# Kernel optimization log

Hardware: AMD Instinct MI355X
Metric: run time of the kernel (lower is better)

The kernel has to match this reference:

```python
import jax, jax.numpy as jnp
import numpy as np

NUM_HEADS = 16
LN_EPS = 1e-5


def setup_inputs() -> dict:
    key = jax.random.key(0)
    ks = jax.random.split(key, 7)
    B, S, D = 4, 1024, 1024
    s_in = 1.0 / np.sqrt(D)
    return {
        "x": jax.random.normal(ks[0], (B, S, D), dtype=jnp.float32),
        # PyTorch MHA packed in-projection: [3D, D] weight, [3D] bias
        "w_qkv": jax.random.uniform(ks[1], (3 * D, D), dtype=jnp.float32, minval=-s_in, maxval=s_in),
        "b_qkv": jnp.zeros((3 * D,), dtype=jnp.float32),
        "w_out": jax.random.uniform(ks[2], (D, D), dtype=jnp.float32, minval=-s_in, maxval=s_in),
        "b_out": jnp.zeros((D,), dtype=jnp.float32),
        "ln_w": jnp.ones((D,), dtype=jnp.float32),
        "ln_b": jnp.zeros((D,), dtype=jnp.float32),
    }


def _layernorm(x, w, b):
    m = jnp.mean(x, axis=-1, keepdims=True)
    v = jnp.var(x, axis=-1, keepdims=True)
    return (x - m) * jax.lax.rsqrt(v + LN_EPS) * w + b


def reference(x, w_qkv, b_qkv, w_out, b_out, ln_w, ln_b):
    B, S, D = x.shape
    H = NUM_HEADS
    hd = D // H
    # packed QKV projection (torch: F.linear(x, w_qkv, b_qkv) then chunk)
    qkv = x @ w_qkv.T + b_qkv                      # [B, S, 3D]
    q, k, v = jnp.split(qkv, 3, axis=-1)
    q = q.reshape(B, S, H, hd).transpose(0, 2, 1, 3) * (hd ** -0.5)  # [B,H,S,hd]
    k = k.reshape(B, S, H, hd).transpose(0, 2, 1, 3)
    v = v.reshape(B, S, H, hd).transpose(0, 2, 1, 3)
    scores = jnp.einsum('bhqd,bhkd->bhqk', q, k)   # [B,H,S,S]
    attn = jax.nn.softmax(scores, axis=-1)
    ctx = jnp.einsum('bhqk,bhkd->bhqd', attn, v)   # [B,H,S,hd]
    ctx = ctx.transpose(0, 2, 1, 3).reshape(B, S, D)
    attn_out = ctx @ w_out.T + b_out
    # torch returns head-averaged weights (average_attn_weights=True)
    attn_weights = attn.mean(axis=1)               # [B,S,S]
    # dropout rate 0.0 -> identity; residual + LayerNorm
    y = _layernorm(x + attn_out, ln_w, ln_b)
    return y, attn_weights
```

## Files before the change

kernel.cpp:

```cpp
#include <hip/hip_runtime.h>
#include <cstdint>

typedef __bf16 bf16;
typedef __bf16 bf16x8 __attribute__((ext_vector_type(8)));
typedef __bf16 bf16x4 __attribute__((ext_vector_type(4)));
typedef float  f32x4  __attribute__((ext_vector_type(4)));

#define MFMA_BF16(a, b, c) __builtin_amdgcn_mfma_f32_16x16x32_bf16(a, b, c, 0, 0, 0)

#define WAITCNT_VM(n) asm volatile("s_waitcnt vmcnt(" #n ")" ::: "memory")
#define CFENCE()      asm volatile("" ::: "memory")

__device__ __forceinline__ void async_load16(const void* g, void* l) {
    __builtin_amdgcn_global_load_lds(
        (__attribute__((address_space(1))) uint32_t*)(uintptr_t)g,
        (__attribute__((address_space(3))) uint32_t*)(uint32_t)(uintptr_t)l,
        16, 0, 0);
}

__global__ void cvt3_kernel(const float* __restrict__ s0, bf16* __restrict__ d0, int n0,
                            const float* __restrict__ s1, bf16* __restrict__ d1, int n1) {
    int i = blockIdx.x * blockDim.x + threadIdx.x;
    const float* s; bf16* d; int j = i;
    if (j < n0) { s = s0; d = d0; }
    else { j -= n0; if (j >= n1) return; s = s1; d = d1; }
    float4 v = ((const float4*)s)[j];
    bf16x4 o;
    o[0] = (bf16)v.x; o[1] = (bf16)v.y; o[2] = (bf16)v.z; o[3] = (bf16)v.w;
    ((bf16x4*)d)[j] = o;
}

__global__ __launch_bounds__(256) void gemm_qkv_kernel(
    const bf16* __restrict__ A, const bf16* __restrict__ W,
    const float* __restrict__ bias,
    bf16* __restrict__ Qb, bf16* __restrict__ Kb, bf16* __restrict__ Vt)
{
    const int Kd = 1024;
    __shared__ __attribute__((aligned(16))) bf16 smem[6 * 128 * 32];
    bf16* const sA0 = smem;
    bf16* const sB0 = smem + 3 * 4096;
    int tid = threadIdx.x, lane = tid & 63, wid = tid >> 6;
    int flat = blockIdx.y * 24 + blockIdx.x;
    int xcd = flat & 7, local = flat >> 3;
    int n0 = (xcd * 3 + local % 3) * 128;
    int m0 = (local / 3) * 128;
    int srow = wid * 32 + (lane >> 2);
    int pchunk = lane & 3;
    int jchunk = pchunk ^ ((lane >> 3) & 3);
    const bf16* Ag = A + (size_t)(m0 + srow) * Kd + jchunk * 8;
    const bf16* Wg = W + (size_t)(n0 + srow) * Kd + jchunk * 8;
    int soff = srow * 32 + pchunk * 8;
    int wm = (wid & 1) * 64, wn = (wid >> 1) * 64;
    int lcol = lane & 15, quad = lane >> 4;
    int ckey = (lcol >> 1) & 3;
    f32x4 acc[4][4] = {};
#define STG_Q(buf, k0_) do { \
        async_load16(Ag + (k0_), sA0 + (buf) * 4096 + soff); \
        async_load16(Ag + (k0_) + 16 * Kd, sA0 + (buf) * 4096 + soff + 512); \
        async_load16(Wg + (k0_), sB0 + (buf) * 4096 + soff); \
        async_load16(Wg + (k0_) + 16 * Kd, sB0 + (buf) * 4096 + soff + 512); \
    } while (0)
    STG_Q(0, 0);
    STG_Q(1, 32);
    STG_Q(2, 64);
    int cur = 0;
    for (int it = 0; it < 32; ++it) {
        if (it < 30)      { WAITCNT_VM(8); }
        else if (it == 30){ WAITCNT_VM(4); }
        else              { WAITCNT_VM(0); }
        __builtin_amdgcn_s_barrier();
        CFENCE();
        const bf16* cA = sA0 + cur * 4096;
        const bf16* cB = sB0 + cur * 4096;
        bf16x8 af[4], bfr[4];
#pragma unroll
        for (int i = 0; i < 4; i++)
            af[i] = *(const bf16x8*)&cA[(wm + i * 16 + lcol) * 32 + (quad ^ ckey) * 8];
#pragma unroll
        for (int i = 0; i < 4; i++)
            bfr[i] = *(const bf16x8*)&cB[(wn + i * 16 + lcol) * 32 + (quad ^ ckey) * 8];
#pragma unroll
        for (int i = 0; i < 4; i++)
#pragma unroll
            for (int j = 0; j < 4; j++)
                acc[i][j] = MFMA_BF16(af[i], bfr[j], acc[i][j]);
        CFENCE();
        __builtin_amdgcn_s_barrier();
        if (it + 3 < 32) STG_Q(cur, (it + 3) * 32);
        cur = (cur == 2) ? 0 : cur + 1;
    }
#undef STG_Q
    const int LP = 136;
    bf16* sE = smem;
    int part = n0 >> 10;
    int h0 = (n0 & 1023) >> 6;
    int b = m0 >> 10, s0 = m0 & 1023;
    if (part == 2) {
#pragma unroll
        for (int j = 0; j < 4; j++) {
            float bv = bias[n0 + wn + j * 16 + lcol];
#pragma unroll
            for (int i = 0; i < 4; i++)
#pragma unroll
                for (int r = 0; r < 4; r++)
                    sE[(wn + j * 16 + lcol) * LP + (wm + i * 16 + quad * 4 + r)] = (bf16)(acc[i][j][r] + bv);
        }
        __syncthreads();
#pragma unroll
        for (int p = 0; p < 8; p++) {
            int c = p * 256 + tid;
            int nl = c >> 4, mc = (c & 15) * 8;
            int dd = nl & 63, h = h0 + (nl >> 6);
            *(bf16x8*)&Vt[(size_t)((b * 16 + h) * 64 + dd) * 1024 + s0 + mc] = *(const bf16x8*)&sE[nl * LP + mc];
        }
    } else {
        float scv = (part == 0) ? 0.125f : 1.0f;
        bf16* dst = (part == 0) ? Qb : Kb;
#pragma unroll
        for (int j = 0; j < 4; j++) {
            float bv = bias[n0 + wn + j * 16 + lcol];
#pragma unroll
            for (int i = 0; i < 4; i++)
#pragma unroll
                for (int r = 0; r < 4; r++)
                    sE[(wm + i * 16 + quad * 4 + r) * LP + (wn + j * 16 + lcol)] = (bf16)((acc[i][j][r] + bv) * scv);
        }
        __syncthreads();
#pragma unroll
        for (int p = 0; p < 8; p++) {
            int c = p * 256 + tid;
            int half = c >> 10, idx = c & 1023;
            int m = idx >> 3, nc = (idx & 7) * 8;
            *(bf16x8*)&dst[(size_t)((b * 16 + h0 + half) * 1024 + s0 + m) * 64 + nc] =
                *(const bf16x8*)&sE[m * LP + half * 64 + nc];
        }
    }
}

__global__ __launch_bounds__(512) void flash_kernel(
    const bf16* __restrict__ Qb, const bf16* __restrict__ Kb, const bf16* __restrict__ Vt,
    bf16* __restrict__ ctx, float* __restrict__ ml,
    const float* __restrict__ wof, bf16* __restrict__ wob)
{
    __shared__ bf16 sK[2][64 * 64];
    __shared__ bf16 sV[2][64 * 64];
    __shared__ bf16 pt[8][16 * 64];
    int tid = threadIdx.x, lane = tid & 63, wid = tid >> 6;
    int bx = blockIdx.x;
    if (bx >= 512) {
        int i = (bx - 512) * 512 + tid;
        float4 v = ((const float4*)wof)[i];
        bf16x4 o;
        o[0] = (bf16)v.x; o[1] = (bf16)v.y; o[2] = (bf16)v.z; o[3] = (bf16)v.w;
        ((bf16x4*)wob)[i] = o;
        return;
    }
    int orig = (bx & 7) * 64 + (bx >> 3);
    int qt = orig & 7;
    int h = (orig >> 3) & 15;
    int b = orig >> 7;
    int lcol = lane & 15, quad = lane >> 4;
    size_t base = (size_t)(b * 16 + h) * 65536;

    int q0 = qt * 128 + wid * 16;
    const bf16* qp = Qb + base + (size_t)(q0 + lcol) * 64 + quad * 8;
    bf16x8 a0 = *(const bf16x8*)qp;
    bf16x8 a1 = *(const bf16x8*)(qp + 32);

    char* wpt = (char*)&pt[wid][0];
    int sr = tid >> 3;
    int pp = tid & 7;
    int jj = pp ^ (sr & 7);
    int sw = lcol & 7;

#define STAGE_KV(buf, kt_) do { \
        async_load16(Kb + base + (size_t)((kt_) * 64 + sr) * 64 + jj * 8, &sK[buf][sr * 64 + pp * 8]); \
        async_load16(Vt + base + (size_t)sr * 1024 + (kt_) * 64 + jj * 8, &sV[buf][sr * 64 + pp * 8]); \
    } while (0)

    float l_[4] = {0.f, 0.f, 0.f, 0.f};
    f32x4 o[4] = {};

    STAGE_KV(0, 0);
    int cur = 0;
    for (int kt = 0; kt < 16; kt++) {
        __syncthreads();
        if (kt < 15) STAGE_KV(cur ^ 1, kt + 1);
        const bf16* sKc = &sK[cur][0];
        const bf16* sVc = &sV[cur][0];
#pragma unroll
        for (int nt = 0; nt < 4; nt++) {
            int ck = quad ^ sw;
            bf16x8 bk0 = *(const bf16x8*)&sKc[(nt * 16 + lcol) * 64 + ck * 8];
            bf16x8 bk1 = *(const bf16x8*)&sKc[(nt * 16 + lcol) * 64 + (ck ^ 4) * 8];
            f32x4 s = {};
            s = MFMA_BF16(a0, bk0, s);
            s = MFMA_BF16(a1, bk1, s);
#pragma unroll
            for (int rr = 0; rr < 4; rr++) {
                float p = __expf(s[rr]);
                l_[rr] += p;
                int row = quad * 4 + rr;
                *(bf16*)(wpt + row * 128 + ((nt * 32 + lcol * 2) ^ ((row & 7) << 4))) = (bf16)p;
            }
        }
#pragma unroll
        for (int kf = 0; kf < 2; kf++) {
            bf16x8 pa = *(const bf16x8*)(wpt + lcol * 128 + (((kf * 4 + quad) ^ sw) << 4));
#pragma unroll
            for (int dt = 0; dt < 4; dt++) {
                bf16x8 vb = *(const bf16x8*)&sVc[(dt * 16 + lcol) * 64 + ((kf * 4 + quad) ^ sw) * 8];
                o[dt] = MFMA_BF16(pa, vb, o[dt]);
            }
        }
        cur ^= 1;
    }
#undef STAGE_KV
#pragma unroll
    for (int mk = 1; mk < 16; mk <<= 1)
#pragma unroll
        for (int rr = 0; rr < 4; rr++) l_[rr] += __shfl_xor(l_[rr], mk, 64);
#pragma unroll
    for (int rr = 0; rr < 4; rr++) {
        float inv = 1.f / l_[rr];
        int row = quad * 4 + rr;
#pragma unroll
        for (int dt = 0; dt < 4; dt++)
            *(bf16*)(wpt + row * 128 + ((dt * 32 + lcol * 2) ^ ((row & 7) << 4))) = (bf16)(o[dt][rr] * inv);
        if (lcol == 0)
            ml[(size_t)(b * 16 + h) * 1024 + q0 + row] = l_[rr];
    }
    int r8a = lane >> 3, ca = lane & 7;
#pragma unroll
    for (int half = 0; half < 2; half++) {
        int r8 = r8a + half * 8;
        bf16x8 v = *(const bf16x8*)(wpt + r8 * 128 + ((ca * 16) ^ ((r8 & 7) << 4)));
        *(bf16x8*)&ctx[(size_t)(b * 1024 + q0 + r8) * 1024 + h * 64 + ca * 8] = v;
    }
}

__global__ __launch_bounds__(512) void awo_kernel(
    const bf16* __restrict__ Qb, const bf16* __restrict__ Kb,
    const float* __restrict__ ml, float* __restrict__ aw,
    const bf16* __restrict__ ctx, const bf16* __restrict__ wob,
    const float* __restrict__ bias, float* __restrict__ yao)
{
    __shared__ __attribute__((aligned(16))) bf16 smem[6 * 128 * 32];
    int tid = threadIdx.x, lane = tid & 63, wid = tid >> 6;
    int bx = blockIdx.x;
    int lcol = lane & 15, quad = lane >> 4;

    if (bx >= 512) {
        const int Kd = 1024;
        bf16* const sA0 = smem;
        bf16* const sB0 = smem + 3 * 4096;
        int obx = bx - 512;
        int m0 = (obx >> 3) * 128, n0 = (obx & 7) * 128;
        int srow = tid >> 2;
        int pchunk = tid & 3;
        int jchunk = pchunk ^ ((tid >> 3) & 3);
        const bf16* Ag = ctx + (size_t)(m0 + srow) * Kd + jchunk * 8;
        const bf16* Wg = wob + (size_t)(n0 + srow) * Kd + jchunk * 8;
        int soff = srow * 32 + pchunk * 8;
        int wm = (wid & 3) * 32, wn = (wid >> 2) * 64;
        int ckey = (lcol >> 1) & 3;
        f32x4 acc[2][4] = {};
#define STG_O(buf, k0_) do { \
        async_load16(Ag + (k0_), sA0 + (buf) * 4096 + soff); \
        async_load16(Wg + (k0_), sB0 + (buf) * 4096 + soff); \
    } while (0)
        STG_O(0, 0);
        STG_O(1, 32);
        STG_O(2, 64);
        int cur = 0;
        for (int it = 0; it < 32; ++it) {
            if (it < 30)      { WAITCNT_VM(4); }
            else if (it == 30){ WAITCNT_VM(2); }
            else              { WAITCNT_VM(0); }
            __builtin_amdgcn_s_barrier();
            CFENCE();
            const bf16* cA = sA0 + cur * 4096;
            const bf16* cB = sB0 + cur * 4096;
            bf16x8 af[2], bfr[4];
#pragma unroll
            for (int i = 0; i < 2; i++)
                af[i] = *(const bf16x8*)&cA[(wm + i * 16 + lcol) * 32 + (quad ^ ckey) * 8];
#pragma unroll
            for (int j = 0; j < 4; j++)
                bfr[j] = *(const bf16x8*)&cB[(wn + j * 16 + lcol) * 32 + (quad ^ ckey) * 8];
#pragma unroll
            for (int i = 0; i < 2; i++)
#pragma unroll
                for (int j = 0; j < 4; j++)
                    acc[i][j] = MFMA_BF16(af[i], bfr[j], acc[i][j]);
            CFENCE();
            __builtin_amdgcn_s_barrier();
            if (it + 3 < 32) STG_O(cur, (it + 3) * 32);
            cur = (cur == 2) ? 0 : cur + 1;
        }
#undef STG_O
#pragma unroll
        for (int j = 0; j < 4; j++) {
            int n = n0 + wn + j * 16 + lcol;
            float bv = bias[n];
#pragma unroll
            for (int i = 0; i < 2; i++) {
                int m = m0 + wm + i * 16 + quad * 4;
#pragma unroll
                for (int r = 0; r < 4; r++) yao[(size_t)(m + r) * 1024 + n] = acc[i][j][r] + bv;
            }
        }
        return;
    }

    bf16* const sK0 = smem;
    int orig = (bx & 7) * 64 + (bx >> 3);
    int kt = orig & 15;
    int qt = (orig >> 4) & 7;
    int b = orig >> 7;
    int q0 = qt * 128 + wid * 16;
    int kbase = kt * 64;
    int sw = lcol & 7;
    int sr = tid >> 3, pp = tid & 7, jj = pp ^ (sr & 7);

#define STAGE_K(buf, hh) \
        async_load16(Kb + (size_t)(b * 16 + (hh)) * 65536 + (size_t)(kbase + sr) * 64 + jj * 8, \
                     sK0 + (buf) * 4096 + sr * 64 + pp * 8)

    float acc[16];
#pragma unroll
    for (int i = 0; i < 16; i++) acc[i] = 0.f;

    bf16x8 a0c, a1c, a0n, a1n;
    float4 mvC, mvN;
    {
        const bf16* qp = Qb + (size_t)(b * 16) * 65536 + (size_t)(q0 + lcol) * 64 + quad * 8;
        a0c = *(const bf16x8*)qp;
        a1c = *(const bf16x8*)(qp + 32);
        mvC = *(const float4*)(ml + (size_t)(b * 16) * 1024 + q0 + quad * 4);
    }
    STAGE_K(0, 0);
    int cur = 0;
    for (int h = 0; h < 16; h++) {
        __syncthreads();
        if (h < 15) {
            STAGE_K(cur ^ 1, h + 1);
            const bf16* qp = Qb + (size_t)(b * 16 + h + 1) * 65536 + (size_t)(q0 + lcol) * 64 + quad * 8;
            a0n = *(const bf16x8*)qp;
            a1n = *(const bf16x8*)(qp + 32);
            mvN = *(const float4*)(ml + (size_t)(b * 16 + h + 1) * 1024 + q0 + quad * 4);
        }
        float scale[4] = {0.0625f / mvC.x, 0.0625f / mvC.y, 0.0625f / mvC.z, 0.0625f / mvC.w};
        const bf16* sKc = sK0 + cur * 4096;
#pragma unroll
        for (int nt = 0; nt < 4; nt++) {
            int ck = quad ^ sw;
            bf16x8 bk0 = *(const bf16x8*)&sKc[(nt * 16 + lcol) * 64 + ck * 8];
            bf16x8 bk1 = *(const bf16x8*)&sKc[(nt * 16 + lcol) * 64 + (ck ^ 4) * 8];
            f32x4 s = {};
            s = MFMA_BF16(a0c, bk0, s);
            s = MFMA_BF16(a1c, bk1, s);
#pragma unroll
            for (int rr = 0; rr < 4; rr++)
                acc[nt * 4 + rr] += __expf(s[rr]) * scale[rr];
        }
        if (h < 15) { a0c = a0n; a1c = a1n; mvC = mvN; }
        cur ^= 1;
    }
#undef STAGE_K
#pragma unroll
    for (int nt = 0; nt < 4; nt++)
#pragma unroll
        for (int rr = 0; rr < 4; rr++)
            aw[(size_t)(b * 1024 + q0 + quad * 4 + rr) * 1024 + kbase + nt * 16 + lcol] = acc[nt * 4 + rr];
}

__global__ __launch_bounds__(256) void ln_kernel(
    const float* __restrict__ x, const float* __restrict__ ao,
    const float* __restrict__ w, const float* __restrict__ bsh,
    float* __restrict__ y)
{
    int row = blockIdx.x, tid = threadIdx.x;
    float4 xv = ((const float4*)(x + (size_t)row * 1024))[tid];
    float4 av = ((const float4*)(ao + (size_t)row * 1024))[tid];
    float4 v = {xv.x + av.x, xv.y + av.y, xv.z + av.z, xv.w + av.w};
    float s = v.x + v.y + v.z + v.w;
    float ss = v.x * v.x + v.y * v.y + v.z * v.z + v.w * v.w;
#pragma unroll
    for (int off = 32; off; off >>= 1) { s += __shfl_down(s, off); ss += __shfl_down(ss, off); }
    __shared__ float rs[4], rss[4];
    int lane = tid & 63, wid = tid >> 6;
    if (lane == 0) { rs[wid] = s; rss[wid] = ss; }
    __syncthreads();
    s = rs[0] + rs[1] + rs[2] + rs[3];
    ss = rss[0] + rss[1] + rss[2] + rss[3];
    float mean = s * (1.f / 1024.f);
    float var = ss * (1.f / 1024.f) - mean * mean;
    float inv = rsqrtf(var + 1e-5f);
    float4 wv = ((const float4*)w)[tid];
    float4 bv = ((const float4*)bsh)[tid];
    float4 o;
    o.x = (v.x - mean) * inv * wv.x + bv.x;
    o.y = (v.y - mean) * inv * wv.y + bv.y;
    o.z = (v.z - mean) * inv * wv.z + bv.z;
    o.w = (v.w - mean) * inv * wv.w + bv.w;
    ((float4*)y)[row * 256 + tid] = o;
}

extern "C" void kernel_launch(void* const* d_in, const int* in_sizes, int n_in,
                              void* d_out, int out_size, void* d_ws, size_t ws_size,
                              hipStream_t stream) {
    const float* x     = (const float*)d_in[0];
    const float* w_qkv = (const float*)d_in[1];
    const float* b_qkv = (const float*)d_in[2];
    const float* w_out = (const float*)d_in[3];
    const float* b_out = (const float*)d_in[4];
    const float* ln_w  = (const float*)d_in[5];
    const float* ln_b  = (const float*)d_in[6];

    char* ws = (char*)d_ws;
    bf16*   Qb    = (bf16*)(ws);
    bf16*   Kb    = (bf16*)(ws + (8ull  << 20));
    bf16*   Vt    = (bf16*)(ws + (16ull << 20));
    bf16*   ctx   = (bf16*)(ws + (24ull << 20));
    float*  ml    = (float*)(ws + (32ull << 20));
    bf16*   x_bf  = (bf16*)(ws + (33ull << 20));
    bf16*   wq_bf = (bf16*)(ws + (41ull << 20));
    bf16*   wo_bf = (bf16*)(ws + (33ull << 20));

    float* y_out  = (float*)d_out;
    float* aw_out = y_out + 4ull * 1024 * 1024;
    float* ao     = y_out;

    cvt3_kernel<<<7168, 256, 0, stream>>>(x, x_bf, 1048576, w_qkv, wq_bf, 786432);
    gemm_qkv_kernel<<<dim3(24, 32), 256, 0, stream>>>(x_bf, wq_bf, b_qkv, Qb, Kb, Vt);
    flash_kernel<<<1024, 512, 0, stream>>>(Qb, Kb, Vt, ctx, ml, w_out, wo_bf);
    awo_kernel<<<768, 512, 0, stream>>>(Qb, Kb, ml, aw_out, ctx, wo_bf, b_out, ao);
    ln_kernel<<<4096, 256, 0, stream>>>(x, ao, ln_w, ln_b, y_out);
}
```

Before: 192.8 us.

## Double block size to 1024 threads in flash and awo kernels

Flash and attention-weight/out-projection kernels now launch 1024-thread blocks covering 256 query rows, so each staged K/V tile is reused by twice as many waves. K and V staging is split between thread halves. The out-projection GEMM branch keeps 128x128 tiles but spreads them over 16 waves with 32x32 per-wave subtiles, and its wait counts are adjusted to match. Fewer blocks and larger per-block register and LDS demand may lower occupancy and reduce scheduling flexibility.

Result: slower. 203.5 us (+5.5%).

```diff
diff --git a/kernel.cpp b/kernel.cpp
--- a/kernel.cpp
+++ b/kernel.cpp
@@ -137,45 +137,46 @@
     }
 }
 
-__global__ __launch_bounds__(512) void flash_kernel(
+__global__ __launch_bounds__(1024) void flash_kernel(
     const bf16* __restrict__ Qb, const bf16* __restrict__ Kb, const bf16* __restrict__ Vt,
     bf16* __restrict__ ctx, float* __restrict__ ml,
     const float* __restrict__ wof, bf16* __restrict__ wob)
 {
     __shared__ bf16 sK[2][64 * 64];
     __shared__ bf16 sV[2][64 * 64];
-    __shared__ bf16 pt[8][16 * 64];
+    __shared__ bf16 pt[16][16 * 64];
     int tid = threadIdx.x, lane = tid & 63, wid = tid >> 6;
     int bx = blockIdx.x;
-    if (bx >= 512) {
-        int i = (bx - 512) * 512 + tid;
+    if (bx >= 256) {
+        int i = (bx - 256) * 1024 + tid;
         float4 v = ((const float4*)wof)[i];
         bf16x4 o;
         o[0] = (bf16)v.x; o[1] = (bf16)v.y; o[2] = (bf16)v.z; o[3] = (bf16)v.w;
         ((bf16x4*)wob)[i] = o;
         return;
     }
-    int orig = (bx & 7) * 64 + (bx >> 3);
-    int qt = orig & 7;
-    int h = (orig >> 3) & 15;
-    int b = orig >> 7;
+    int orig = (bx & 7) * 32 + (bx >> 3);
+    int qt = orig & 3;
+    int h = (orig >> 2) & 15;
+    int b = orig >> 6;
     int lcol = lane & 15, quad = lane >> 4;
     size_t base = (size_t)(b * 16 + h) * 65536;
 
-    int q0 = qt * 128 + wid * 16;
+    int q0 = qt * 256 + wid * 16;
     const bf16* qp = Qb + base + (size_t)(q0 + lcol) * 64 + quad * 8;
     bf16x8 a0 = *(const bf16x8*)qp;
     bf16x8 a1 = *(const bf16x8*)(qp + 32);
 
     char* wpt = (char*)&pt[wid][0];
-    int sr = tid >> 3;
-    int pp = tid & 7;
+    int st = tid & 511;
+    int sr = st >> 3;
+    int pp = st & 7;
     int jj = pp ^ (sr & 7);
     int sw = lcol & 7;
 
 #define STAGE_KV(buf, kt_) do { \
-        async_load16(Kb + base + (size_t)((kt_) * 64 + sr) * 64 + jj * 8, &sK[buf][sr * 64 + pp * 8]); \
-        async_load16(Vt + base + (size_t)sr * 1024 + (kt_) * 64 + jj * 8, &sV[buf][sr * 64 + pp * 8]); \
+        if (tid < 512) async_load16(Kb + base + (size_t)((kt_) * 64 + sr) * 64 + jj * 8, &sK[buf][sr * 64 + pp * 8]); \
+        else           async_load16(Vt + base + (size_t)sr * 1024 + (kt_) * 64 + jj * 8, &sV[buf][sr * 64 + pp * 8]); \
     } while (0)
 
     float l_[4] = {0.f, 0.f, 0.f, 0.f};
@@ -239,7 +240,7 @@
     }
 }
 
-__global__ __launch_bounds__(512) void awo_kernel(
+__global__ __launch_bounds__(1024) void awo_kernel(
     const bf16* __restrict__ Qb, const bf16* __restrict__ Kb,
     const float* __restrict__ ml, float* __restrict__ aw,
     const bf16* __restrict__ ctx, const bf16* __restrict__ wob,
@@ -250,48 +251,48 @@
     int bx = blockIdx.x;
     int lcol = lane & 15, quad = lane >> 4;
 
-    if (bx >= 512) {
+    if (bx >= 256) {
         const int Kd = 1024;
         bf16* const sA0 = smem;
         bf16* const sB0 = smem + 3 * 4096;
-        int obx = bx - 512;
+        int obx = bx - 256;
         int m0 = (obx >> 3) * 128, n0 = (obx & 7) * 128;
-        int srow = tid >> 2;
-        int pchunk = tid & 3;
-        int jchunk = pchunk ^ ((tid >> 3) & 3);
-        const bf16* Ag = ctx + (size_t)(m0 + srow) * Kd + jchunk * 8;
-        const bf16* Wg = wob + (size_t)(n0 + srow) * Kd + jchunk * 8;
+        int st = tid & 511;
+        int srow = st >> 2;
+        int pchunk = st & 3;
+        int jchunk = pchunk ^ ((st >> 3) & 3);
         int soff = srow * 32 + pchunk * 8;
-        int wm = (wid & 3) * 32, wn = (wid >> 2) * 64;
+        const bf16* Gsrc = (tid < 512)
+            ? ctx + (size_t)(m0 + srow) * Kd + jchunk * 8
+            : wob + (size_t)(n0 + srow) * Kd + jchunk * 8;
+        bf16* const Ldst0 = (tid < 512) ? sA0 + soff : sB0 + soff;
+        int wm = (wid & 3) * 32, wn = (wid >> 2) * 32;
         int ckey = (lcol >> 1) & 3;
-        f32x4 acc[2][4] = {};
-#define STG_O(buf, k0_) do { \
-        async_load16(Ag + (k0_), sA0 + (buf) * 4096 + soff); \
-        async_load16(Wg + (k0_), sB0 + (buf) * 4096 + soff); \
-    } while (0)
+        f32x4 acc[2][2] = {};
+#define STG_O(buf, k0_) async_load16(Gsrc + (k0_), Ldst0 + (buf) * 4096)
         STG_O(0, 0);
         STG_O(1, 32);
         STG_O(2, 64);
         int cur = 0;
         for (int it = 0; it < 32; ++it) {
-            if (it < 30)      { WAITCNT_VM(4); }
-            else if (it == 30){ WAITCNT_VM(2); }
+            if (it < 30)      { WAITCNT_VM(2); }
+            else if (it == 30){ WAITCNT_VM(1); }
             else              { WAITCNT_VM(0); }
             __builtin_amdgcn_s_barrier();
             CFENCE();
             const bf16* cA = sA0 + cur * 4096;
             const bf16* cB = sB0 + cur * 4096;
-            bf16x8 af[2], bfr[4];
+            bf16x8 af[2], bfr[2];
 #pragma unroll
             for (int i = 0; i < 2; i++)
                 af[i] = *(const bf16x8*)&cA[(wm + i * 16 + lcol) * 32 + (quad ^ ckey) * 8];
 #pragma unroll
-            for (int j = 0; j < 4; j++)
+            for (int j = 0; j < 2; j++)
                 bfr[j] = *(const bf16x8*)&cB[(wn + j * 16 + lcol) * 32 + (quad ^ ckey) * 8];
 #pragma unroll
             for (int i = 0; i < 2; i++)
 #pragma unroll
-                for (int j = 0; j < 4; j++)
+                for (int j = 0; j < 2; j++)
                     acc[i][j] = MFMA_BF16(af[i], bfr[j], acc[i][j]);
             CFENCE();
             __builtin_amdgcn_s_barrier();
@@ -300,7 +301,7 @@
         }
 #undef STG_O
 #pragma unroll
-        for (int j = 0; j < 4; j++) {
+        for (int j = 0; j < 2; j++) {
             int n = n0 + wn + j * 16 + lcol;
             float bv = bias[n];
 #pragma unroll
@@ -314,18 +315,20 @@
     }
 
     bf16* const sK0 = smem;
-    int orig = (bx & 7) * 64 + (bx >> 3);
+    int orig = (bx & 7) * 32 + (bx >> 3);
     int kt = orig & 15;
-    int qt = (orig >> 4) & 7;
-    int b = orig >> 7;
-    int q0 = qt * 128 + wid * 16;
+    int qt = (orig >> 4) & 3;
+    int b = orig >> 6;
+    int q0 = qt * 256 + wid * 16;
     int kbase = kt * 64;
     int sw = lcol & 7;
     int sr = tid >> 3, pp = tid & 7, jj = pp ^ (sr & 7);
 
-#define STAGE_K(buf, hh) \
-        async_load16(Kb + (size_t)(b * 16 + (hh)) * 65536 + (size_t)(kbase + sr) * 64 + jj * 8, \
-                     sK0 + (buf) * 4096 + sr * 64 + pp * 8)
+#define STAGE_K(buf, hh) do { \
+        if (tid < 512) \
+            async_load16(Kb + (size_t)(b * 16 + (hh)) * 65536 + (size_t)(kbase + sr) * 64 + jj * 8, \
+                         sK0 + (buf) * 4096 + sr * 64 + pp * 8); \
+    } while (0)
 
     float acc[16];
 #pragma unroll
@@ -434,7 +437,7 @@
 
     cvt3_kernel<<<7168, 256, 0, stream>>>(x, x_bf, 1048576, w_qkv, wq_bf, 786432);
     gemm_qkv_kernel<<<dim3(24, 32), 256, 0, stream>>>(x_bf, wq_bf, b_qkv, Qb, Kb, Vt);
-    flash_kernel<<<1024, 512, 0, stream>>>(Qb, Kb, Vt, ctx, ml, w_out, wo_bf);
-    awo_kernel<<<768, 512, 0, stream>>>(Qb, Kb, ml, aw_out, ctx, wo_bf, b_out, ao);
+    flash_kernel<<<512, 1024, 0, stream>>>(Qb, Kb, Vt, ctx, ml, w_out, wo_bf);
+    awo_kernel<<<512, 1024, 0, stream>>>(Qb, Kb, ml, aw_out, ctx, wo_bf, b_out, ao);
     ln_kernel<<<4096, 256, 0, stream>>>(x, ao, ln_w, ln_b, y_out);
 }
```
